# Kernel optimization log

Hardware: AMD Instinct MI355X
Metric: run time of the kernel (lower is better)

## Reference

```python
import jax, jax.numpy as jnp
import numpy as np

# BilateralFilter(d=5, sigmaColor=0.1, sigmaSpace=1) ~ skimage.restoration.denoise_bilateral
# win_size=5 -> radius 2; mode='constant', cval=0 (skimage default) -> zero padding,
# padded zeros participate in the weighted average like skimage's constant mode.
WIN_RADIUS = 2          # d=5 -> (5-1)//2
SIGMA_COLOR = 0.1       # range Gaussian std (image in [0,1])
SIGMA_SPATIAL = 1.0     # spatial Gaussian std


def setup_inputs() -> dict:
    key = jax.random.key(0)
    # batch of [0,1] RGB images, as produced by skimage's img_as_float on uint8 PIL images
    x = jax.random.uniform(key, (16, 512, 512, 3), dtype=jnp.float32)
    return {"x": x}


def _bilateral(x):
    B, H, W, C = x.shape
    R = WIN_RADIUS
    inv2_sc = 1.0 / (SIGMA_COLOR * SIGMA_COLOR)
    inv2_ss = 1.0 / (SIGMA_SPATIAL * SIGMA_SPATIAL)
    padded = jnp.pad(x, ((0, 0), (R, R), (R, R), (0, 0)))  # constant-zero, like skimage default
    num = jnp.zeros_like(x)                  # [B,H,W,C] weighted sum
    den = jnp.zeros(x.shape[:-1], x.dtype)   # [B,H,W]   weight sum
    # fixed 5x5 = 25 offsets; loop over small constant window, fully vectorized over B,H,W,C
    for dy in range(-R, R + 1):
        for dx in range(-R, R + 1):
            nbr = jax.lax.dynamic_slice(padded, (0, R + dy, R + dx, 0), (B, H, W, C))
            # squared Euclidean color distance across channels
            cdist2 = jnp.sum((nbr - x) ** 2, axis=-1)  # [B,H,W]
            # w = exp(-0.5*(d_spatial/sigma_s)^2) * exp(-0.5*(d_color/sigma_c)^2)
            w = jnp.exp(-0.5 * ((dy * dy + dx * dx) * inv2_ss + cdist2 * inv2_sc))
            num = num + w[..., None] * nbr
            den = den + w
    return num / den[..., None]  # center weight is 1, so den >= 1


def reference(x) -> jnp.ndarray:
    return _bilateral(x)
```

## Files before the change

### kernel.cpp

```cpp
#include <hip/hip_runtime.h>

#define LOG2E 1.4426950408889634f
#define NEG50L (-50.0f * LOG2E)
#define M100L (100.0f * LOG2E)

#define B_ 16
#define H_ 512
#define W_ 512

#define TILE_C 64
#define TH 2
#define TILE_R 8
#define LR (TILE_R + 4)
#define LC (TILE_C + 4)
#define NTEX (LR * LC)

#define EXP2(x) __builtin_amdgcn_exp2f(x)

typedef float f4 __attribute__((ext_vector_type(4)));
typedef float f3 __attribute__((ext_vector_type(3), aligned(4)));
typedef float f2 __attribute__((ext_vector_type(2)));

__device__ __forceinline__ constexpr int sidx(int sd) {
    return (sd == 0) ? 0 : (sd == 1) ? 1 : (sd == 2) ? 2
         : (sd == 4) ? 3 : (sd == 5) ? 4 : 5;
}

__global__ __launch_bounds__(256) void bilateral_kernel(
    const float* __restrict__ x, float* __restrict__ out)
{
    __shared__ f4 tile[NTEX];
    __shared__ float tileq[NTEX];

    const int bid = blockIdx.x;
    const int ct = bid & 7;
    const int rt = (bid >> 3) & 63;
    const int b0 = bid >> 9;
    const int c0 = ct * TILE_C;
    const int h0 = rt * TILE_R;

    const float* __restrict__ img = x + (size_t)b0 * (H_ * W_ * 3);
    float* __restrict__ oimg      = out + (size_t)b0 * (H_ * W_ * 3);

#pragma unroll
    for (int k = 0; k < 4; ++k) {
        const int s = threadIdx.x + k * 256;
        if (k < 3 || s < NTEX) {
            const int lr = s / LC;
            const int lc = s - lr * LC;
            const int gr = h0 - 2 + lr;
            const int gc = c0 - 2 + lc;
            const int cr_ = min(max(gr, 0), H_ - 1);
            const int cc_ = min(max(gc, 0), W_ - 1);
            const bool ok = (gr == cr_) && (gc == cc_);
            const f3 v = *(const f3*)(img + (cr_ * W_ + cc_) * 3);
            f4 t;
            t.x = ok ? v.x : 0.0f;
            t.y = ok ? v.y : 0.0f;
            t.z = ok ? v.z : 0.0f;
            t.w = 1.0f;
            float n2 = t.x * t.x;
            n2 = fmaf(t.y, t.y, n2);
            n2 = fmaf(t.z, t.z, n2);
            tile[s] = t;
            tileq[s] = NEG50L * n2;
        }
    }
    __syncthreads();

    const int lane  = threadIdx.x & 63;
    const int wv    = threadIdx.x >> 6;
    const int rbase = wv * TH;

    float kc[TH][3], qsp[TH][6];
    f2 accRG[TH], accB1[TH];
#pragma unroll
    for (int j = 0; j < TH; ++j) {
        const int ci = (rbase + j + 2) * LC + (lane + 2);
        const f4 c = tile[ci];
        const float qc = tileq[ci];
        kc[j][0] = M100L * c.x;
        kc[j][1] = M100L * c.y;
        kc[j][2] = M100L * c.z;
        qsp[j][0] = qc;
        qsp[j][1] = qc + (-0.5f * LOG2E) * 1.0f;
        qsp[j][2] = qc + (-0.5f * LOG2E) * 2.0f;
        qsp[j][3] = qc + (-0.5f * LOG2E) * 4.0f;
        qsp[j][4] = qc + (-0.5f * LOG2E) * 5.0f;
        qsp[j][5] = qc + (-0.5f * LOG2E) * 8.0f;
        accRG[j] = (f2){c.x, c.y};
        accB1[j] = (f2){c.z, 1.0f};
    }

#pragma unroll
    for (int r = 0; r < TH + 4; ++r) {
        f4 row[5];
        float rowq[5];
#pragma unroll
        for (int dx = 0; dx < 5; ++dx) {
            const int ti = (rbase + r) * LC + (lane + dx);
            row[dx] = tile[ti];
            rowq[dx] = tileq[ti];
        }

#pragma unroll
        for (int j = 0; j < TH; ++j) {
            if (r - j >= 0 && r - j <= 4) {
                const int dy = r - j;
                const int sdy = (dy - 2) * (dy - 2);
#pragma unroll
                for (int dx = 0; dx < 5; ++dx) {
                    if (dy == 2 && dx == 2) continue;
                    const f4 n = row[dx];
                    float s = fmaf(n.x, kc[j][0], rowq[dx]);
                    s = fmaf(n.y, kc[j][1], s);
                    s = fmaf(n.z, kc[j][2], s);
                    const int si = sidx(sdy + (dx - 2) * (dx - 2));
                    const float arg = s + qsp[j][si];
                    const float w = EXP2(arg);
                    const f2 w2 = {w, w};
                    const f2 nRG = {n.x, n.y};
                    const f2 nB1 = {n.z, n.w};
                    accRG[j] = __builtin_elementwise_fma(w2, nRG, accRG[j]);
                    accB1[j] = __builtin_elementwise_fma(w2, nB1, accB1[j]);
                }
            }
        }
    }

#pragma unroll
    for (int j = 0; j < TH; ++j) {
        const float inv = __builtin_amdgcn_rcpf(accB1[j].y);
        float* op = oimg + ((size_t)(h0 + rbase + j) * W_ + (c0 + lane)) * 3;
        op[0] = accRG[j].x * inv;
        op[1] = accRG[j].y * inv;
        op[2] = accB1[j].x * inv;
    }
}

extern "C" void kernel_launch(void* const* d_in, const int* in_sizes, int n_in,
                              void* d_out, int out_size, void* d_ws, size_t ws_size,
                              hipStream_t stream) {
    const float* x = (const float*)d_in[0];
    float* out = (float*)d_out;

    const int grid = B_ * (W_ / TILE_C) * (H_ / TILE_R);
    const int block = 256;

    bilateral_kernel<<<grid, block, 0, stream>>>(x, out);
}
```

Before: 37.78 us.

## Make blocks persistent over four row tiles with register prefetch of the next tile

```diff
diff --git a/kernel.cpp b/kernel.cpp
--- a/kernel.cpp
+++ b/kernel.cpp
@@ -11,6 +11,7 @@
 #define TILE_C 64
 #define TH 2
 #define TILE_R 8
+#define KSTEP 4
 #define LR (TILE_R + 4)
 #define LC (TILE_C + 4)
 #define NTEX (LR * LC)
@@ -34,107 +35,126 @@
 
     const int bid = blockIdx.x;
     const int ct = bid & 7;
-    const int rt = (bid >> 3) & 63;
-    const int b0 = bid >> 9;
+    const int st = (bid >> 3) & 15;
+    const int b0 = bid >> 7;
     const int c0 = ct * TILE_C;
-    const int h0 = rt * TILE_R;
+    const int H0 = st * (TILE_R * KSTEP);
 
     const float* __restrict__ img = x + (size_t)b0 * (H_ * W_ * 3);
     float* __restrict__ oimg      = out + (size_t)b0 * (H_ * W_ * 3);
-
-#pragma unroll
-    for (int k = 0; k < 4; ++k) {
-        const int s = threadIdx.x + k * 256;
-        if (k < 3 || s < NTEX) {
-            const int lr = s / LC;
-            const int lc = s - lr * LC;
-            const int gr = h0 - 2 + lr;
-            const int gc = c0 - 2 + lc;
-            const int cr_ = min(max(gr, 0), H_ - 1);
-            const int cc_ = min(max(gc, 0), W_ - 1);
-            const bool ok = (gr == cr_) && (gc == cc_);
-            const f3 v = *(const f3*)(img + (cr_ * W_ + cc_) * 3);
-            f4 t;
-            t.x = ok ? v.x : 0.0f;
-            t.y = ok ? v.y : 0.0f;
-            t.z = ok ? v.z : 0.0f;
-            t.w = 1.0f;
-            float n2 = t.x * t.x;
-            n2 = fmaf(t.y, t.y, n2);
-            n2 = fmaf(t.z, t.z, n2);
-            tile[s] = t;
-            tileq[s] = NEG50L * n2;
-        }
-    }
-    __syncthreads();
 
     const int lane  = threadIdx.x & 63;
     const int wv    = threadIdx.x >> 6;
     const int rbase = wv * TH;
 
-    float kc[TH][3], qsp[TH][6];
-    f2 accRG[TH], accB1[TH];
+    f3 pf[4];
+    auto prefetch = [&](int h0) {
 #pragma unroll
-    for (int j = 0; j < TH; ++j) {
-        const int ci = (rbase + j + 2) * LC + (lane + 2);
-        const f4 c = tile[ci];
-        const float qc = tileq[ci];
-        kc[j][0] = M100L * c.x;
-        kc[j][1] = M100L * c.y;
-        kc[j][2] = M100L * c.z;
-        qsp[j][0] = qc;
-        qsp[j][1] = qc + (-0.5f * LOG2E) * 1.0f;
-        qsp[j][2] = qc + (-0.5f * LOG2E) * 2.0f;
-        qsp[j][3] = qc + (-0.5f * LOG2E) * 4.0f;
-        qsp[j][4] = qc + (-0.5f * LOG2E) * 5.0f;
-        qsp[j][5] = qc + (-0.5f * LOG2E) * 8.0f;
-        accRG[j] = (f2){c.x, c.y};
-        accB1[j] = (f2){c.z, 1.0f};
-    }
+        for (int i = 0; i < 4; ++i) {
+            const int s = (int)threadIdx.x + i * 256;
+            if (i < 3 || s < NTEX) {
+                const int lr = s / LC;
+                const int lc = s - lr * LC;
+                const int gr = h0 - 2 + lr;
+                const int gc = c0 - 2 + lc;
+                const int cr_ = min(max(gr, 0), H_ - 1);
+                const int cc_ = min(max(gc, 0), W_ - 1);
+                const bool ok = (gr == cr_) && (gc == cc_);
+                const f3 v = *(const f3*)(img + (cr_ * W_ + cc_) * 3);
+                pf[i].x = ok ? v.x : 0.0f;
+                pf[i].y = ok ? v.y : 0.0f;
+                pf[i].z = ok ? v.z : 0.0f;
+            }
+        }
+    };
+
+    prefetch(H0);
+
+#pragma unroll 1
+    for (int s = 0; s < KSTEP; ++s) {
+        const int h0 = H0 + s * TILE_R;
+
+        __syncthreads();
+#pragma unroll
+        for (int i = 0; i < 4; ++i) {
+            const int si = (int)threadIdx.x + i * 256;
+            if (i < 3 || si < NTEX) {
+                f4 t;
+                t.x = pf[i].x; t.y = pf[i].y; t.z = pf[i].z;
+                t.w = 1.0f;
+                float n2 = t.x * t.x;
+                n2 = fmaf(t.y, t.y, n2);
+                n2 = fmaf(t.z, t.z, n2);
+                tile[si] = t;
+                tileq[si] = NEG50L * n2;
+            }
+        }
+        if (s < KSTEP - 1) prefetch(h0 + TILE_R);
+        __syncthreads();
+
+        float kc[TH][3], qsp[TH][6];
+        f2 accRG[TH], accB1[TH];
+#pragma unroll
+        for (int j = 0; j < TH; ++j) {
+            const int ci = (rbase + j + 2) * LC + (lane + 2);
+            const f4 c = tile[ci];
+            const float qc = tileq[ci];
+            kc[j][0] = M100L * c.x;
+            kc[j][1] = M100L * c.y;
+            kc[j][2] = M100L * c.z;
+            qsp[j][0] = qc;
+            qsp[j][1] = qc + (-0.5f * LOG2E) * 1.0f;
+            qsp[j][2] = qc + (-0.5f * LOG2E) * 2.0f;
+            qsp[j][3] = qc + (-0.5f * LOG2E) * 4.0f;
+            qsp[j][4] = qc + (-0.5f * LOG2E) * 5.0f;
+            qsp[j][5] = qc + (-0.5f * LOG2E) * 8.0f;
+            accRG[j] = (f2){c.x, c.y};
+            accB1[j] = (f2){c.z, 1.0f};
+        }
 
 #pragma unroll
-    for (int r = 0; r < TH + 4; ++r) {
-        f4 row[5];
-        float rowq[5];
+        for (int r = 0; r < TH + 4; ++r) {
+            f4 row[5];
+            float rowq[5];
 #pragma unroll
-        for (int dx = 0; dx < 5; ++dx) {
-            const int ti = (rbase + r) * LC + (lane + dx);
-            row[dx] = tile[ti];
-            rowq[dx] = tileq[ti];
+            for (int dx = 0; dx < 5; ++dx) {
+                const int ti = (rbase + r) * LC + (lane + dx);
+                row[dx] = tile[ti];
+                rowq[dx] = tileq[ti];
+            }
+#pragma unroll
+            for (int j = 0; j < TH; ++j) {
+                if (r - j >= 0 && r - j <= 4) {
+                    const int dy = r - j;
+                    const int sdy = (dy - 2) * (dy - 2);
+#pragma unroll
+                    for (int dx = 0; dx < 5; ++dx) {
+                        if (dy == 2 && dx == 2) continue;
+                        const f4 n = row[dx];
+                        float sD = fmaf(n.x, kc[j][0], rowq[dx]);
+                        sD = fmaf(n.y, kc[j][1], sD);
+                        sD = fmaf(n.z, kc[j][2], sD);
+                        const int si2 = sidx(sdy + (dx - 2) * (dx - 2));
+                        const float arg = sD + qsp[j][si2];
+                        const float w = EXP2(arg);
+                        const f2 w2 = {w, w};
+                        const f2 nRG = {n.x, n.y};
+                        const f2 nB1 = {n.z, n.w};
+                        accRG[j] = __builtin_elementwise_fma(w2, nRG, accRG[j]);
+                        accB1[j] = __builtin_elementwise_fma(w2, nB1, accB1[j]);
+                    }
+                }
+            }
         }
 
 #pragma unroll
         for (int j = 0; j < TH; ++j) {
-            if (r - j >= 0 && r - j <= 4) {
-                const int dy = r - j;
-                const int sdy = (dy - 2) * (dy - 2);
-#pragma unroll
-                for (int dx = 0; dx < 5; ++dx) {
-                    if (dy == 2 && dx == 2) continue;
-                    const f4 n = row[dx];
-                    float s = fmaf(n.x, kc[j][0], rowq[dx]);
-                    s = fmaf(n.y, kc[j][1], s);
-                    s = fmaf(n.z, kc[j][2], s);
-                    const int si = sidx(sdy + (dx - 2) * (dx - 2));
-                    const float arg = s + qsp[j][si];
-                    const float w = EXP2(arg);
-                    const f2 w2 = {w, w};
-                    const f2 nRG = {n.x, n.y};
-                    const f2 nB1 = {n.z, n.w};
-                    accRG[j] = __builtin_elementwise_fma(w2, nRG, accRG[j]);
-                    accB1[j] = __builtin_elementwise_fma(w2, nB1, accB1[j]);
-                }
-            }
+            const float inv = __builtin_amdgcn_rcpf(accB1[j].y);
+            float* op = oimg + ((size_t)(h0 + rbase + j) * W_ + (c0 + lane)) * 3;
+            op[0] = accRG[j].x * inv;
+            op[1] = accRG[j].y * inv;
+            op[2] = accB1[j].x * inv;
         }
-    }
-
-#pragma unroll
-    for (int j = 0; j < TH; ++j) {
-        const float inv = __builtin_amdgcn_rcpf(accB1[j].y);
-        float* op = oimg + ((size_t)(h0 + rbase + j) * W_ + (c0 + lane)) * 3;
-        op[0] = accRG[j].x * inv;
-        op[1] = accRG[j].y * inv;
-        op[2] = accB1[j].x * inv;
     }
 }
 
@@ -144,7 +164,7 @@
     const float* x = (const float*)d_in[0];
     float* out = (float*)d_out;
 
-    const int grid = B_ * (W_ / TILE_C) * (H_ / TILE_R);
+    const int grid = B_ * (W_ / TILE_C) * (H_ / (TILE_R * KSTEP));
     const int block = 256;
 
     bilateral_kernel<<<grid, block, 0, stream>>>(x, out);
```

Result: slower. 39.71 us (+5.1%).

## Compute two adjacent columns per thread with wider tile and vectorized stores

Applied to the files above, without the earlier changes.

```diff
diff --git a/kernel.cpp b/kernel.cpp
--- a/kernel.cpp
+++ b/kernel.cpp
@@ -8,7 +8,8 @@
 #define H_ 512
 #define W_ 512
 
-#define TILE_C 64
+#define TILE_C 128
+#define CW 2
 #define TH 2
 #define TILE_R 8
 #define LR (TILE_R + 4)
@@ -18,13 +19,10 @@
 #define EXP2(x) __builtin_amdgcn_exp2f(x)
 
 typedef float f4 __attribute__((ext_vector_type(4)));
+typedef float f4u __attribute__((ext_vector_type(4), aligned(4)));
 typedef float f3 __attribute__((ext_vector_type(3), aligned(4)));
 typedef float f2 __attribute__((ext_vector_type(2)));
-
-__device__ __forceinline__ constexpr int sidx(int sd) {
-    return (sd == 0) ? 0 : (sd == 1) ? 1 : (sd == 2) ? 2
-         : (sd == 4) ? 3 : (sd == 5) ? 4 : 5;
-}
+typedef float f2u __attribute__((ext_vector_type(2), aligned(4)));
 
 __global__ __launch_bounds__(256) void bilateral_kernel(
     const float* __restrict__ x, float* __restrict__ out)
@@ -33,9 +31,9 @@
     __shared__ float tileq[NTEX];
 
     const int bid = blockIdx.x;
-    const int ct = bid & 7;
-    const int rt = (bid >> 3) & 63;
-    const int b0 = bid >> 9;
+    const int ct = bid & 3;
+    const int rt = (bid >> 2) & 63;
+    const int b0 = bid >> 8;
     const int c0 = ct * TILE_C;
     const int h0 = rt * TILE_R;
 
@@ -43,13 +41,13 @@
     float* __restrict__ oimg      = out + (size_t)b0 * (H_ * W_ * 3);
 
 #pragma unroll
-    for (int k = 0; k < 4; ++k) {
-        const int s = threadIdx.x + k * 256;
-        if (k < 3 || s < NTEX) {
+    for (int k = 0; k < 7; ++k) {
+        const int s = (int)threadIdx.x + k * 256;
+        if (k < 6 || s < NTEX) {
             const int lr = s / LC;
-            const int lc = s - lr * LC;
+            const int lc_ = s - lr * LC;
             const int gr = h0 - 2 + lr;
-            const int gc = c0 - 2 + lc;
+            const int gc = c0 - 2 + lc_;
             const int cr_ = min(max(gr, 0), H_ - 1);
             const int cc_ = min(max(gc, 0), W_ - 1);
             const bool ok = (gr == cr_) && (gc == cc_);
@@ -71,37 +69,35 @@
     const int lane  = threadIdx.x & 63;
     const int wv    = threadIdx.x >> 6;
     const int rbase = wv * TH;
+    const int cb    = lane * CW;
 
-    float kc[TH][3], qsp[TH][6];
-    f2 accRG[TH], accB1[TH];
+    float kc[TH][CW][3], qc[TH][CW];
+    f2 accRG[TH][CW], accB1[TH][CW];
 #pragma unroll
-    for (int j = 0; j < TH; ++j) {
-        const int ci = (rbase + j + 2) * LC + (lane + 2);
-        const f4 c = tile[ci];
-        const float qc = tileq[ci];
-        kc[j][0] = M100L * c.x;
-        kc[j][1] = M100L * c.y;
-        kc[j][2] = M100L * c.z;
-        qsp[j][0] = qc;
-        qsp[j][1] = qc + (-0.5f * LOG2E) * 1.0f;
-        qsp[j][2] = qc + (-0.5f * LOG2E) * 2.0f;
-        qsp[j][3] = qc + (-0.5f * LOG2E) * 4.0f;
-        qsp[j][4] = qc + (-0.5f * LOG2E) * 5.0f;
-        qsp[j][5] = qc + (-0.5f * LOG2E) * 8.0f;
-        accRG[j] = (f2){c.x, c.y};
-        accB1[j] = (f2){c.z, 1.0f};
-    }
+    for (int j = 0; j < TH; ++j)
+#pragma unroll
+        for (int cc = 0; cc < CW; ++cc) {
+            const int ci = (rbase + j + 2) * LC + (cb + 2 + cc);
+            const f4 c = tile[ci];
+            kc[j][cc][0] = M100L * c.x;
+            kc[j][cc][1] = M100L * c.y;
+            kc[j][cc][2] = M100L * c.z;
+            qc[j][cc] = tileq[ci];
+            accRG[j][cc] = (f2){c.x, c.y};
+            accB1[j][cc] = (f2){c.z, 1.0f};
+        }
 
 #pragma unroll
     for (int r = 0; r < TH + 4; ++r) {
-        f4 row[5];
-        float rowq[5];
+        const int tb = (rbase + r) * LC + cb;
+        f4 row[6];
+        float rowq[6];
 #pragma unroll
-        for (int dx = 0; dx < 5; ++dx) {
-            const int ti = (rbase + r) * LC + (lane + dx);
-            row[dx] = tile[ti];
-            rowq[dx] = tileq[ti];
-        }
+        for (int d = 0; d < 6; ++d)
+            row[d] = tile[tb + d];
+#pragma unroll
+        for (int d = 0; d < 3; ++d)
+            *(f2*)&rowq[2 * d] = *(const f2*)&tileq[tb + 2 * d];
 
 #pragma unroll
         for (int j = 0; j < TH; ++j) {
@@ -109,20 +105,26 @@
                 const int dy = r - j;
                 const int sdy = (dy - 2) * (dy - 2);
 #pragma unroll
-                for (int dx = 0; dx < 5; ++dx) {
-                    if (dy == 2 && dx == 2) continue;
-                    const f4 n = row[dx];
-                    float s = fmaf(n.x, kc[j][0], rowq[dx]);
-                    s = fmaf(n.y, kc[j][1], s);
-                    s = fmaf(n.z, kc[j][2], s);
-                    const int si = sidx(sdy + (dx - 2) * (dx - 2));
-                    const float arg = s + qsp[j][si];
-                    const float w = EXP2(arg);
-                    const f2 w2 = {w, w};
-                    const f2 nRG = {n.x, n.y};
-                    const f2 nB1 = {n.z, n.w};
-                    accRG[j] = __builtin_elementwise_fma(w2, nRG, accRG[j]);
-                    accB1[j] = __builtin_elementwise_fma(w2, nB1, accB1[j]);
+                for (int cc = 0; cc < CW; ++cc) {
+#pragma unroll
+                    for (int dx = 0; dx < 5; ++dx) {
+                        if (dy == 2 && dx == 2) continue;
+                        const f4 n = row[cc + dx];
+                        float s = fmaf(n.x, kc[j][cc][0], rowq[cc + dx]);
+                        s = fmaf(n.y, kc[j][cc][1], s);
+                        s = fmaf(n.z, kc[j][cc][2], s);
+                        const float sp = -0.5f * LOG2E *
+                            (float)(sdy + (dx - 2) * (dx - 2));
+                        const float arg = (s + qc[j][cc]) + sp;
+                        const float w = EXP2(arg);
+                        const f2 w2 = {w, w};
+                        const f2 nRG = {n.x, n.y};
+                        const f2 nB1 = {n.z, n.w};
+                        accRG[j][cc] =
+                            __builtin_elementwise_fma(w2, nRG, accRG[j][cc]);
+                        accB1[j][cc] =
+                            __builtin_elementwise_fma(w2, nB1, accB1[j][cc]);
+                    }
                 }
             }
         }
@@ -130,11 +132,15 @@
 
 #pragma unroll
     for (int j = 0; j < TH; ++j) {
-        const float inv = __builtin_amdgcn_rcpf(accB1[j].y);
-        float* op = oimg + ((size_t)(h0 + rbase + j) * W_ + (c0 + lane)) * 3;
-        op[0] = accRG[j].x * inv;
-        op[1] = accRG[j].y * inv;
-        op[2] = accB1[j].x * inv;
+        const float inv0 = __builtin_amdgcn_rcpf(accB1[j][0].y);
+        const float inv1 = __builtin_amdgcn_rcpf(accB1[j][1].y);
+        float* op = oimg +
+            ((size_t)(h0 + rbase + j) * W_ + (c0 + cb)) * 3;
+        f4u v0 = {accRG[j][0].x * inv0, accRG[j][0].y * inv0,
+                  accB1[j][0].x * inv0, accRG[j][1].x * inv1};
+        f2u v1 = {accRG[j][1].y * inv1, accB1[j][1].x * inv1};
+        *(f4u*)op = v0;
+        *(f2u*)(op + 4) = v1;
     }
 }
 
```

Result: slower. 47.48 us (+25.7%).
